# Optimization experiments

Measured on AMD Instinct MI355X. Metric: run time of the kernel, lower is better.

The kernel has to match this reference:

```python
import jax, jax.numpy as jnp
import numpy as np
import math

B, N, T, F_IN, F_OUT = 8, 512, 12, 32, 64


def setup_inputs() -> dict:
    key = jax.random.key(0)
    k1, k2, k3, k4, k5 = jax.random.split(key, 5)
    x = jax.random.normal(k1, (B, N, T, F_IN), dtype=jnp.float32)
    phaseAct_matrix = jax.random.uniform(k2, (B, T, N, N), dtype=jnp.float32)
    adj = jax.random.uniform(k3, (N, N), dtype=jnp.float32)  # sym-normalized adjacency stand-in
    mask = (jax.random.uniform(k4, (N,)) < 0.5).astype(jnp.float32)  # 1 = observed node, 0 = unknown
    theta = jax.random.normal(k5, (F_IN, F_OUT), dtype=jnp.float32) * 0.05
    return {"x": x, "phaseAct_matrix": phaseAct_matrix, "adj": adj, "mask": mask, "theta": theta}


def _spatial_attention(x):
    # x: (B, N, T, F) -> scores (B, T, N, N)
    f = x.shape[-1]
    xt = x.transpose(0, 2, 1, 3)  # (B, T, N, F)
    score = jnp.einsum('btnf,btmf->btnm', xt, xt) / math.sqrt(f)
    return jax.nn.softmax(score, axis=-1)


def reference(x, phaseAct_matrix, adj, mask, theta):
    f = x.shape[-1]
    t_steps = x.shape[2]
    inv_sqrt_f = 1.0 / math.sqrt(f)
    m = mask[None, :, None, None]  # broadcast over (B, N, T-1, F)

    def body(i, x_cur):
        sa = _spatial_attention(x_cur) * inv_sqrt_f          # (B, T, N, N)
        sat_act = (phaseAct_matrix * sa).transpose(0, 1, 3, 2)  # (B, T, N, N) transposed
        xt = x_cur.transpose(0, 2, 1, 3)                     # (B, T, N, F)
        # predict step t from step t-1: (B, T-1, N, F)
        x_pred = jnp.einsum('btnm,btmf->btnf', sat_act[:, 1:], xt[:, :t_steps - 1])
        x_pred = x_pred.transpose(0, 2, 1, 3)                # (B, N, T-1, F)
        # revise_unknown: keep observed nodes, impute unknown nodes at steps 1..T-1
        x_rev = x_cur[:, :, 1:, :] * m + x_pred * (1.0 - m)
        return jnp.concatenate([x_cur[:, :, 0:1, :], x_rev], axis=2)

    x = jax.lax.fori_loop(1, t_steps, body, x)

    sa = _spatial_attention(x) * inv_sqrt_f                  # (B, T, N, N)
    satAct_adj = phaseAct_matrix * adj[None, None] * sa      # (B, T, N, N)
    xt = x.transpose(0, 2, 1, 3)                             # (B, T, N, F)
    agg = jnp.einsum('btmn,btmf->btnf', satAct_adj, xt)      # transpose(adj) @ x
    out = jax.nn.relu(jnp.einsum('btnf,fo->btno', agg, theta))  # (B, T, N, F_out)
    return out.transpose(0, 2, 1, 3)                         # (B, N, T, F_out)
```

## Files before the change

kernel.cpp:

```cpp
#include <hip/hip_runtime.h>


#define B_ 8
#define N_ 512
#define T_ 12
#define F_ 32
#define O_ 64
#define MT 4
#define NW 8

typedef unsigned int uint_t;
typedef unsigned short ushort_t;
typedef _Float16 f16_t;
typedef _Float16 f16x4 __attribute__((ext_vector_type(4)));
typedef _Float16 f16x8 __attribute__((ext_vector_type(8)));
typedef float f32x4 __attribute__((ext_vector_type(4)));

__device__ __forceinline__ void atomAddF(float* p, float v) {
    __hip_atomic_fetch_add(p, v, __ATOMIC_RELAXED, __HIP_MEMORY_SCOPE_AGENT);
}
__device__ __forceinline__ int xidx(int b, int n, int t, int f) {
    return ((b * N_ + n) * T_ + t) * F_ + f;
}
__device__ __forceinline__ f16x8 load_frag8(const float* p) {
    float4 a = *reinterpret_cast<const float4*>(p);
    float4 b = *reinterpret_cast<const float4*>(p + 4);
    f16x8 r;
    r[0] = (f16_t)a.x; r[1] = (f16_t)a.y; r[2] = (f16_t)a.z; r[3] = (f16_t)a.w;
    r[4] = (f16_t)b.x; r[5] = (f16_t)b.y; r[6] = (f16_t)b.z; r[7] = (f16_t)b.w;
    return r;
}
union U2H4 { uint2 u; f16x4 h; };

__global__ __launch_bounds__(256)
void permute_kernel(const float* __restrict__ src, ushort_t* __restrict__ dst)
{
    __shared__ float Lp[16][516];
    const int tid = threadIdx.x;
    const int mc  = blockIdx.x;
    const int s   = blockIdx.y;
    src += (size_t)s * N_ * N_ + (size_t)mc * 16 * N_;
    uint_t* dstu = (uint_t*)dst + (size_t)s * 131072 + (size_t)mc * 4096;

    #pragma unroll
    for (int k = 0; k < 32; ++k) {
        int idx = tid + 256 * k;
        Lp[idx >> 9][idx & 511] = src[idx];
    }
    __syncthreads();
    #pragma unroll
    for (int k = 0; k < 16; ++k) {
        int u    = tid + 256 * k;
        int nt   = u >> 7;
        int r    = u & 127;
        int quad = r >> 5;
        int cl   = (r >> 1) & 15;
        int m0   = quad * 4 + (r & 1) * 2;
        int n    = nt * 16 + cl;
        union { f16_t h[2]; uint_t i; } pk;
        pk.h[0] = (f16_t)Lp[m0][n];
        pk.h[1] = (f16_t)Lp[m0 + 1][n];
        dstu[u] = pk.i;
    }
}

template <int FINAL>
__global__ __launch_bounds__(512)
void gcn_kernel(const float* __restrict__ x0,
                const float* __restrict__ xcur,
                float* __restrict__ dst,
                const ushort_t* __restrict__ phase_h,
                const ushort_t* __restrict__ adj_h,
                const float* __restrict__ mask)
{
    __shared__ float2 st[2][NW][16];

    const int tid  = threadIdx.x;
    const int w    = tid >> 6;
    const int l    = tid & 63;
    const int quad = l >> 4;
    const int col  = l & 15;
    const int mt   = blockIdx.x;
    const int t    = FINAL ? blockIdx.y : blockIdx.y + 1;
    const int b    = blockIdx.z;
    const int nt0  = w * 4;
    const float inv_f = 0.17677669529663687f;

    const float* xs     = (FINAL && t == 0) ? x0 : xcur;
    const float* xp_src = FINAL ? xs : ((t == 1) ? x0 : xcur);
    const int    tp     = FINAL ? t : t - 1;

    f16x8 bf[4];
    #pragma unroll
    for (int i = 0; i < 4; ++i)
        bf[i] = load_frag8(&xs[xidx(b, (nt0 + i) * 16 + col, t, quad * 8)]);

    f32x4 acc[4][2];
    #pragma unroll
    for (int i = 0; i < 4; ++i) {
        acc[i][0] = (f32x4){0.f, 0.f, 0.f, 0.f};
        acc[i][1] = (f32x4){0.f, 0.f, 0.f, 0.f};
    }

    const uint_t* phu = (const uint_t*)phase_h + (size_t)(b * T_ + t) * 131072;
    const uint_t* adu = (const uint_t*)adj_h;

    for (int c = 0; c < 512 / (MT * 16); ++c) {
        const int mb = mt * (N_ / MT) + c * 16;
        const int mc = mb >> 4;

        f16x8 af = load_frag8(&xs[xidx(b, mb + col, t, quad * 8)]);
        f32x4 s4[4];
        #pragma unroll
        for (int i = 0; i < 4; ++i) {
            s4[i] = __builtin_amdgcn_mfma_f32_16x16x32_f16(
                        af, bf[i], (f32x4){0.f, 0.f, 0.f, 0.f}, 0, 0, 0);
        }
        float mxw[4], sw[4], e[4][4];
        #pragma unroll
        for (int v = 0; v < 4; ++v) {
            #pragma unroll
            for (int i = 0; i < 4; ++i) s4[i][v] *= inv_f;
            mxw[v] = fmaxf(fmaxf(s4[0][v], s4[1][v]), fmaxf(s4[2][v], s4[3][v]));
        }
        #pragma unroll
        for (int d = 1; d < 16; d <<= 1)
            #pragma unroll
            for (int v = 0; v < 4; ++v)
                mxw[v] = fmaxf(mxw[v], __shfl_xor(mxw[v], d, 64));
        #pragma unroll
        for (int v = 0; v < 4; ++v) {
            #pragma unroll
            for (int i = 0; i < 4; ++i) e[i][v] = __expf(s4[i][v] - mxw[v]);
            sw[v] = (e[0][v] + e[1][v]) + (e[2][v] + e[3][v]);
        }
        #pragma unroll
        for (int d = 1; d < 16; d <<= 1)
            #pragma unroll
            for (int v = 0; v < 4; ++v)
                sw[v] += __shfl_xor(sw[v], d, 64);

        const int buf = c & 1;
        if (col < 4) {
            float mv = (col == 0) ? mxw[0] : (col == 1) ? mxw[1] : (col == 2) ? mxw[2] : mxw[3];
            float sv = (col == 0) ? sw[0]  : (col == 1) ? sw[1]  : (col == 2) ? sw[2]  : sw[3];
            st[buf][w][quad * 4 + col] = make_float2(mv, sv);
        }
        __syncthreads();
        {
            const int row = l >> 2, wp = l & 3;
            float2 p0 = st[buf][2 * wp][row];
            float2 p1 = st[buf][2 * wp + 1][row];
            float M = fmaxf(p0.x, p1.x);
            float S = p0.y * __expf(p0.x - M) + p1.y * __expf(p1.x - M);
            #pragma unroll
            for (int d = 1; d < 4; d <<= 1) {
                float Mo = __shfl_xor(M, d, 64), So = __shfl_xor(S, d, 64);
                float Mn = fmaxf(M, Mo);
                S = S * __expf(M - Mn) + So * __expf(Mo - Mn);
                M = Mn;
            }
            #pragma unroll
            for (int v = 0; v < 4; ++v) {
                float Mr = __shfl(M, quad * 16 + v * 4, 64);
                float Sr = __shfl(S, quad * 16 + v * 4, 64);
                e[0][v] *= 1.f;
                mxw[v] = __expf(mxw[v] - Mr) * inv_f / Sr;
            }
        }

        f16x4 bp[2];
        #pragma unroll
        for (int ft = 0; ft < 2; ++ft)
            #pragma unroll
            for (int j = 0; j < 4; ++j)
                bp[ft][j] = (f16_t)xp_src[xidx(b, mb + quad * 4 + j, tp, ft * 16 + col)];

        #pragma unroll
        for (int i = 0; i < 4; ++i) {
            U2H4 ph; ph.u = *(const uint2*)(phu + (size_t)mc * 4096 + (nt0 + i) * 128 + l * 2);
            f16x4 wf;
            if (FINAL) {
                U2H4 aj; aj.u = *(const uint2*)(adu + (size_t)mc * 4096 + (nt0 + i) * 128 + l * 2);
                #pragma unroll
                for (int v = 0; v < 4; ++v)
                    wf[v] = (f16_t)(e[i][v] * mxw[v] * (float)ph.h[v] * (float)aj.h[v]);
            } else {
                #pragma unroll
                for (int v = 0; v < 4; ++v)
                    wf[v] = (f16_t)(e[i][v] * mxw[v] * (float)ph.h[v]);
            }
            #pragma unroll
            for (int ft = 0; ft < 2; ++ft)
                acc[i][ft] = __builtin_amdgcn_mfma_f32_16x16x16f16(wf, bp[ft], acc[i][ft], 0, 0, 0);
        }
    }

    #pragma unroll
    for (int i = 0; i < 4; ++i) {
        #pragma unroll
        for (int v = 0; v < 4; ++v) {
            const int n = (nt0 + i) * 16 + quad * 4 + v;
            if (FINAL) {
                float* d0 = &dst[((b * T_ + t) * N_ + n) * F_ + col];
                atomAddF(d0, acc[i][0][v]);
                atomAddF(d0 + 16, acc[i][1][v]);
            } else if (mask[n] == 0.f) {
                atomAddF(&dst[xidx(b, n, t, col)], acc[i][0][v]);
                atomAddF(&dst[xidx(b, n, t, 16 + col)], acc[i][1][v]);
            }
        }
    }
    if (!FINAL && mt == 0) {
        for (int p = tid; p < N_ * F_; p += 512) {
            int n = p >> 5, f = p & 31;
            if (mask[n] != 0.f) dst[xidx(b, n, t, f)] = xcur[xidx(b, n, t, f)];
        }
    }
}

__global__ __launch_bounds__(256)
void proj_kernel(const float* __restrict__ agg, const float* __restrict__ theta,
                 float* __restrict__ out)
{
    __shared__ float th[F_ * O_];
    int tid = threadIdx.x;
    #pragma unroll
    for (int p = 0; p < 8; ++p) th[tid + 256 * p] = theta[tid + 256 * p];
    __syncthreads();
    int g  = blockIdx.x * 256 + tid;
    int o  = g & 63;
    int r  = g >> 6;
    int tt = r % T_;
    int r2 = r / T_;
    int n  = r2 & 511;
    int b  = r2 >> 9;
    const float* a = &agg[((b * T_ + tt) * N_ + n) * F_];
    float s = 0.f;
    #pragma unroll
    for (int f = 0; f < F_; ++f) s += a[f] * th[f * O_ + o];
    out[g] = fmaxf(s, 0.f);
}

extern "C" void kernel_launch(void* const* d_in, const int* in_sizes, int n_in,
                              void* d_out, int out_size, void* d_ws, size_t ws_size,
                              hipStream_t stream)
{
    const float* x     = (const float*)d_in[0];
    const float* phase = (const float*)d_in[1];
    const float* adj   = (const float*)d_in[2];
    const float* mask  = (const float*)d_in[3];
    const float* theta = (const float*)d_in[4];
    float* out = (float*)d_out;

    const size_t XE = (size_t)B_ * N_ * T_ * F_;
    float*    xA      = (float*)d_ws;
    float*    xB      = xA + XE;
    float*    agg     = xB + XE;
    ushort_t* phase_h = (ushort_t*)(agg + XE);
    ushort_t* adj_h   = phase_h + (size_t)96 * N_ * N_;

    permute_kernel<<<dim3(32, 96), 256, 0, stream>>>(phase, phase_h);
    permute_kernel<<<dim3(32, 1), 256, 0, stream>>>(adj, adj_h);

    const float* cur = x;
    float* bufs[2] = { xA, xB };
    for (int i = 0; i < T_ - 1; ++i) {
        float* nxt = bufs[i & 1];
        hipMemsetAsync(nxt, 0, XE * sizeof(float), stream);
        gcn_kernel<0><<<dim3(MT, T_ - 1, B_), 512, 0, stream>>>(
            x, cur, nxt, phase_h, adj_h, mask);
        cur = nxt;
    }
    hipMemsetAsync(agg, 0, XE * sizeof(float), stream);
    gcn_kernel<1><<<dim3(MT, T_, B_), 512, 0, stream>>>(
        x, cur, agg, phase_h, adj_h, mask);
    proj_kernel<<<(B_ * N_ * T_ * O_) / 256, 256, 0, stream>>>(agg, theta, out);
}
```

Measured before the change: 893.4 us.

## Drop softmax max pass, prefetch chunks, double split and vectorize atomics

Softmax no longer subtracts a running max. Exponentials are clamped at 60 and only row sums are reduced, via LDS float atomics, which removes the per-chunk cross-wave max/sum merge. The next chunk's x, phase and adj fragments are prefetched during compute, and the node split grows from 4 to 8 blocks. Output accumulation uses packed 2-float global atomics, and the per-iteration memsets are replaced by one upfront memset of eleven separate buffers. Dropping the max shift risks overflow or clamping error if scores ever exceed the clamp, and it needs more workspace.

```diff
diff --git a/kernel.cpp b/kernel.cpp
--- a/kernel.cpp
+++ b/kernel.cpp
@@ -6,8 +6,7 @@
 #define T_ 12
 #define F_ 32
 #define O_ 64
-#define MT 4
-#define NW 8
+#define MT 8
 
 typedef unsigned int uint_t;
 typedef unsigned short ushort_t;
@@ -15,10 +14,25 @@
 typedef _Float16 f16x4 __attribute__((ext_vector_type(4)));
 typedef _Float16 f16x8 __attribute__((ext_vector_type(8)));
 typedef float f32x4 __attribute__((ext_vector_type(4)));
+typedef float f32x2 __attribute__((ext_vector_type(2)));
 
 __device__ __forceinline__ void atomAddF(float* p, float v) {
     __hip_atomic_fetch_add(p, v, __ATOMIC_RELAXED, __HIP_MEMORY_SCOPE_AGENT);
 }
+#if __has_builtin(__builtin_amdgcn_global_atomic_fadd_v2f32)
+typedef __attribute__((address_space(1))) f32x2 f32x2_as1;
+__device__ __forceinline__ void atomAdd2(float* p, float a, float b) {
+    __builtin_amdgcn_global_atomic_fadd_v2f32((f32x2_as1*)(unsigned long long)p,
+                                              (f32x2){a, b});
+}
+#else
+__device__ __forceinline__ void atomAdd2(float* p, float a, float b) {
+    atomAddF(p, a); atomAddF(p + 1, b);
+}
+#endif
+
+#define LGKM_BARRIER() asm volatile("s_waitcnt lgkmcnt(0)\n\ts_barrier" ::: "memory")
+
 __device__ __forceinline__ int xidx(int b, int n, int t, int f) {
     return ((b * N_ + n) * T_ + t) * F_ + f;
 }
@@ -73,7 +87,7 @@
                 const ushort_t* __restrict__ adj_h,
                 const float* __restrict__ mask)
 {
-    __shared__ float2 st[2][NW][16];
+    __shared__ float st[4][16];
 
     const int tid  = threadIdx.x;
     const int w    = tid >> 6;
@@ -86,14 +100,34 @@
     const int nt0  = w * 4;
     const float inv_f = 0.17677669529663687f;
 
-    const float* xs     = (FINAL && t == 0) ? x0 : xcur;
-    const float* xp_src = FINAL ? xs : ((t == 1) ? x0 : xcur);
-    const int    tp     = FINAL ? t : t - 1;
+    const float* xs = (FINAL && t == 0) ? x0 : xcur;
+    const float* xp = FINAL ? xs : ((t == 1) ? x0 : xcur);
+    const int    tp = FINAL ? t : t - 1;
+
+    if (tid < 64) ((float*)st)[tid] = 0.f;
 
     f16x8 bf[4];
     #pragma unroll
     for (int i = 0; i < 4; ++i)
         bf[i] = load_frag8(&xs[xidx(b, (nt0 + i) * 16 + col, t, quad * 8)]);
+
+    const uint_t* phu = (const uint_t*)phase_h + (size_t)(b * T_ + t) * 131072;
+    const uint_t* adu = (const uint_t*)adj_h;
+
+    f16x8 af = load_frag8(&xs[xidx(b, mt * 64 + col, t, quad * 8)]);
+    f16x4 bp[2];
+    #pragma unroll
+    for (int fh = 0; fh < 2; ++fh)
+        #pragma unroll
+        for (int j = 0; j < 4; ++j)
+            bp[fh][j] = (f16_t)xp[xidx(b, mt * 64 + quad * 4 + j, tp, fh * 16 + col)];
+    uint2 ph[4], aj[4];
+    #pragma unroll
+    for (int i = 0; i < 4; ++i) {
+        ph[i] = *(const uint2*)(phu + (size_t)(mt * 4) * 4096 + (nt0 + i) * 128 + l * 2);
+        if (FINAL)
+            aj[i] = *(const uint2*)(adu + (size_t)(mt * 4) * 4096 + (nt0 + i) * 128 + l * 2);
+    }
 
     f32x4 acc[4][2];
     #pragma unroll
@@ -102,36 +136,38 @@
         acc[i][1] = (f32x4){0.f, 0.f, 0.f, 0.f};
     }
 
-    const uint_t* phu = (const uint_t*)phase_h + (size_t)(b * T_ + t) * 131072;
-    const uint_t* adu = (const uint_t*)adj_h;
-
-    for (int c = 0; c < 512 / (MT * 16); ++c) {
-        const int mb = mt * (N_ / MT) + c * 16;
-        const int mc = mb >> 4;
-
-        f16x8 af = load_frag8(&xs[xidx(b, mb + col, t, quad * 8)]);
+    LGKM_BARRIER();
+
+    for (int c = 0; c < 4; ++c) {
         f32x4 s4[4];
         #pragma unroll
-        for (int i = 0; i < 4; ++i) {
+        for (int i = 0; i < 4; ++i)
             s4[i] = __builtin_amdgcn_mfma_f32_16x16x32_f16(
                         af, bf[i], (f32x4){0.f, 0.f, 0.f, 0.f}, 0, 0, 0);
-        }
-        float mxw[4], sw[4], e[4][4];
+
+        const int c2  = (c < 3) ? c + 1 : c;
+        const int mb2 = mt * 64 + c2 * 16;
+        f16x8 af_n = load_frag8(&xs[xidx(b, mb2 + col, t, quad * 8)]);
+        f16x4 bp_n[2];
+        #pragma unroll
+        for (int fh = 0; fh < 2; ++fh)
+            #pragma unroll
+            for (int j = 0; j < 4; ++j)
+                bp_n[fh][j] = (f16_t)xp[xidx(b, mb2 + quad * 4 + j, tp, fh * 16 + col)];
+        uint2 ph_n[4], aj_n[4];
+        #pragma unroll
+        for (int i = 0; i < 4; ++i) {
+            ph_n[i] = *(const uint2*)(phu + (size_t)(mt * 4 + c2) * 4096 + (nt0 + i) * 128 + l * 2);
+            if (FINAL)
+                aj_n[i] = *(const uint2*)(adu + (size_t)(mt * 4 + c2) * 4096 + (nt0 + i) * 128 + l * 2);
+        }
+
+        float e[4][4], sw[4];
         #pragma unroll
         for (int v = 0; v < 4; ++v) {
             #pragma unroll
-            for (int i = 0; i < 4; ++i) s4[i][v] *= inv_f;
-            mxw[v] = fmaxf(fmaxf(s4[0][v], s4[1][v]), fmaxf(s4[2][v], s4[3][v]));
-        }
-        #pragma unroll
-        for (int d = 1; d < 16; d <<= 1)
-            #pragma unroll
-            for (int v = 0; v < 4; ++v)
-                mxw[v] = fmaxf(mxw[v], __shfl_xor(mxw[v], d, 64));
-        #pragma unroll
-        for (int v = 0; v < 4; ++v) {
-            #pragma unroll
-            for (int i = 0; i < 4; ++i) e[i][v] = __expf(s4[i][v] - mxw[v]);
+            for (int i = 0; i < 4; ++i)
+                e[i][v] = __expf(fminf(s4[i][v] * inv_f, 60.f));
             sw[v] = (e[0][v] + e[1][v]) + (e[2][v] + e[3][v]);
         }
         #pragma unroll
@@ -139,75 +175,58 @@
             #pragma unroll
             for (int v = 0; v < 4; ++v)
                 sw[v] += __shfl_xor(sw[v], d, 64);
-
-        const int buf = c & 1;
         if (col < 4) {
-            float mv = (col == 0) ? mxw[0] : (col == 1) ? mxw[1] : (col == 2) ? mxw[2] : mxw[3];
-            float sv = (col == 0) ? sw[0]  : (col == 1) ? sw[1]  : (col == 2) ? sw[2]  : sw[3];
-            st[buf][w][quad * 4 + col] = make_float2(mv, sv);
-        }
-        __syncthreads();
-        {
-            const int row = l >> 2, wp = l & 3;
-            float2 p0 = st[buf][2 * wp][row];
-            float2 p1 = st[buf][2 * wp + 1][row];
-            float M = fmaxf(p0.x, p1.x);
-            float S = p0.y * __expf(p0.x - M) + p1.y * __expf(p1.x - M);
-            #pragma unroll
-            for (int d = 1; d < 4; d <<= 1) {
-                float Mo = __shfl_xor(M, d, 64), So = __shfl_xor(S, d, 64);
-                float Mn = fmaxf(M, Mo);
-                S = S * __expf(M - Mn) + So * __expf(Mo - Mn);
-                M = Mn;
-            }
-            #pragma unroll
-            for (int v = 0; v < 4; ++v) {
-                float Mr = __shfl(M, quad * 16 + v * 4, 64);
-                float Sr = __shfl(S, quad * 16 + v * 4, 64);
-                e[0][v] *= 1.f;
-                mxw[v] = __expf(mxw[v] - Mr) * inv_f / Sr;
-            }
-        }
-
-        f16x4 bp[2];
-        #pragma unroll
-        for (int ft = 0; ft < 2; ++ft)
-            #pragma unroll
-            for (int j = 0; j < 4; ++j)
-                bp[ft][j] = (f16_t)xp_src[xidx(b, mb + quad * 4 + j, tp, ft * 16 + col)];
+            float sv = (col == 0) ? sw[0] : (col == 1) ? sw[1] : (col == 2) ? sw[2] : sw[3];
+            atomicAdd(&st[c][quad * 4 + col], sv);
+        }
 
         #pragma unroll
         for (int i = 0; i < 4; ++i) {
-            U2H4 ph; ph.u = *(const uint2*)(phu + (size_t)mc * 4096 + (nt0 + i) * 128 + l * 2);
-            f16x4 wf;
+            U2H4 P; P.u = ph[i];
             if (FINAL) {
-                U2H4 aj; aj.u = *(const uint2*)(adu + (size_t)mc * 4096 + (nt0 + i) * 128 + l * 2);
+                U2H4 A; A.u = aj[i];
                 #pragma unroll
-                for (int v = 0; v < 4; ++v)
-                    wf[v] = (f16_t)(e[i][v] * mxw[v] * (float)ph.h[v] * (float)aj.h[v]);
+                for (int v = 0; v < 4; ++v) e[i][v] *= (float)P.h[v] * (float)A.h[v];
             } else {
                 #pragma unroll
-                for (int v = 0; v < 4; ++v)
-                    wf[v] = (f16_t)(e[i][v] * mxw[v] * (float)ph.h[v]);
+                for (int v = 0; v < 4; ++v) e[i][v] *= (float)P.h[v];
             }
-            #pragma unroll
-            for (int ft = 0; ft < 2; ++ft)
-                acc[i][ft] = __builtin_amdgcn_mfma_f32_16x16x16f16(wf, bp[ft], acc[i][ft], 0, 0, 0);
-        }
+        }
+
+        LGKM_BARRIER();
+
+        f32x4 rs = *(const f32x4*)&st[c][quad * 4];
+        f32x4 bet;
+        #pragma unroll
+        for (int v = 0; v < 4; ++v) bet[v] = inv_f * __builtin_amdgcn_rcpf(rs[v]);
+        #pragma unroll
+        for (int i = 0; i < 4; ++i) {
+            f16x4 wf;
+            #pragma unroll
+            for (int v = 0; v < 4; ++v) wf[v] = (f16_t)(e[i][v] * bet[v]);
+            #pragma unroll
+            for (int fh = 0; fh < 2; ++fh)
+                acc[i][fh] = __builtin_amdgcn_mfma_f32_16x16x16f16(bp[fh], wf, acc[i][fh], 0, 0, 0);
+        }
+
+        af = af_n;
+        bp[0] = bp_n[0]; bp[1] = bp_n[1];
+        #pragma unroll
+        for (int i = 0; i < 4; ++i) { ph[i] = ph_n[i]; if (FINAL) aj[i] = aj_n[i]; }
     }
 
     #pragma unroll
     for (int i = 0; i < 4; ++i) {
-        #pragma unroll
-        for (int v = 0; v < 4; ++v) {
-            const int n = (nt0 + i) * 16 + quad * 4 + v;
-            if (FINAL) {
-                float* d0 = &dst[((b * T_ + t) * N_ + n) * F_ + col];
-                atomAddF(d0, acc[i][0][v]);
-                atomAddF(d0 + 16, acc[i][1][v]);
-            } else if (mask[n] == 0.f) {
-                atomAddF(&dst[xidx(b, n, t, col)], acc[i][0][v]);
-                atomAddF(&dst[xidx(b, n, t, 16 + col)], acc[i][1][v]);
+        const int n = (nt0 + i) * 16 + col;
+        const bool go = FINAL ? true : (mask[n] == 0.f);
+        if (go) {
+            float* d0 = FINAL ? &dst[((b * T_ + t) * N_ + n) * F_]
+                              : &dst[xidx(b, n, t, 0)];
+            #pragma unroll
+            for (int fh = 0; fh < 2; ++fh) {
+                float* p = d0 + fh * 16 + quad * 4;
+                atomAdd2(p,     acc[i][fh][0], acc[i][fh][1]);
+                atomAdd2(p + 2, acc[i][fh][2], acc[i][fh][3]);
             }
         }
     }
@@ -254,25 +273,22 @@
     float* out = (float*)d_out;
 
     const size_t XE = (size_t)B_ * N_ * T_ * F_;
-    float*    xA      = (float*)d_ws;
-    float*    xB      = xA + XE;
-    float*    agg     = xB + XE;
-    ushort_t* phase_h = (ushort_t*)(agg + XE);
+    float*    bufs    = (float*)d_ws;
+    float*    agg     = bufs + (size_t)11 * XE;
+    ushort_t* phase_h = (ushort_t*)(bufs + (size_t)12 * XE);
     ushort_t* adj_h   = phase_h + (size_t)96 * N_ * N_;
 
+    hipMemsetAsync(bufs, 0, (size_t)12 * XE * sizeof(float), stream);
     permute_kernel<<<dim3(32, 96), 256, 0, stream>>>(phase, phase_h);
     permute_kernel<<<dim3(32, 1), 256, 0, stream>>>(adj, adj_h);
 
     const float* cur = x;
-    float* bufs[2] = { xA, xB };
     for (int i = 0; i < T_ - 1; ++i) {
-        float* nxt = bufs[i & 1];
-        hipMemsetAsync(nxt, 0, XE * sizeof(float), stream);
+        float* nxt = bufs + (size_t)i * XE;
         gcn_kernel<0><<<dim3(MT, T_ - 1, B_), 512, 0, stream>>>(
             x, cur, nxt, phase_h, adj_h, mask);
         cur = nxt;
     }
-    hipMemsetAsync(agg, 0, XE * sizeof(float), stream);
     gcn_kernel<1><<<dim3(MT, T_, B_), 512, 0, stream>>>(
         x, cur, agg, phase_h, adj_h, mask);
     proj_kernel<<<(B_ * N_ * T_ * O_) / 256, 256, 0, stream>>>(agg, theta, out);
```

Result: slower. 1.603 ms (+79.4%).
